# Kernel tuning notes

Measured on AMD Instinct MI355X. Metric: run time of the kernel, lower is better.

Reference implementation:

```python
import jax, jax.numpy as jnp
import numpy as np

B, S, D = 2, 2048, 1024
H, HD = 16, 64
ROPE_BASE = 1000.0


def rope(x):
    # x: [B, H, S, hd]; interleaved (GPT-NeoX-style pairs) rotary embedding, base=1000
    d = x.shape[-1]
    theta = 1.0 / (ROPE_BASE ** (jnp.arange(0, d, 2, dtype=jnp.float32) / d))  # [d/2]
    theta = jnp.repeat(theta, 2)                                               # [d]
    pos = jnp.arange(x.shape[-2], dtype=jnp.float32)                           # [S]
    pm = pos[:, None] * theta[None, :]                                         # [S, d]
    cos, sin = jnp.cos(pm), jnp.sin(pm)
    # rotated: _x[..., 0::2] = -x[..., 1::2]; _x[..., 1::2] = x[..., 0::2]
    rot = jnp.stack([-x[..., 1::2], x[..., 0::2]], axis=-1).reshape(x.shape)
    return x * cos + rot * sin


def setup_inputs() -> dict:
    key = jax.random.key(0)
    ks = jax.random.split(key, 12)
    sc = 1.0 / np.sqrt(D)
    inp = {
        "query": jax.random.normal(ks[0], (B, S, D), jnp.float32),
        "key": jax.random.normal(ks[1], (B, S, D), jnp.float32),
        "value": jax.random.normal(ks[2], (B, S, D), jnp.float32),
        "mask": jnp.broadcast_to(jnp.tril(jnp.ones((S, S), jnp.int32)), (B, S, S)),
        "Wq": jax.random.normal(ks[3], (D, H * HD), jnp.float32) * sc,
        "bq": jax.random.normal(ks[4], (H * HD,), jnp.float32) * 0.01,
        "Wk": jax.random.normal(ks[5], (D, H * HD), jnp.float32) * sc,
        "bk": jax.random.normal(ks[6], (H * HD,), jnp.float32) * 0.01,
        "Wv": jax.random.normal(ks[7], (D, H * HD), jnp.float32) * sc,
        "bv": jax.random.normal(ks[8], (H * HD,), jnp.float32) * 0.01,
        "Wo": jax.random.normal(ks[9], (H * HD, D), jnp.float32) * sc,
        "bo": jax.random.normal(ks[10], (D,), jnp.float32) * 0.01,
    }
    return inp


def reference(query, key, value, mask, Wq, bq, Wk, bk, Wv, bv, Wo, bo):
    b = query.shape[0]
    split = lambda t: t.reshape(b, -1, H, HD).transpose(0, 2, 1, 3)  # [B,H,S,hd]
    q = split(query @ Wq + bq)
    k = split(key @ Wk + bk)
    v = split(value @ Wv + bv)
    qr, kr = rope(q), rope(k)
    scale = jnp.sqrt(jnp.float32(HD))
    num = jnp.exp(jnp.einsum("bhqd,bhkd->bhqk", qr, kr) / scale)           # [B,H,S,S]
    den = jnp.sum(jnp.exp(jnp.einsum("bhqd,bhkd->bhqk", q, k) / scale),
                  axis=-1, keepdims=True)                                   # [B,H,S,1]
    a = num / den
    a = jnp.where(mask[:, None, :, :] == 0, -jnp.inf, a)
    alpha = jax.nn.softmax(a, axis=-1)
    z = jnp.einsum("bhqk,bhkd->bhqd", alpha, v)
    z = z.transpose(0, 2, 1, 3).reshape(b, -1, H * HD)
    return z @ Wo + bo
```

## Files before the change

### kernel.cpp

```cpp
#include <hip/hip_runtime.h>


#define Bn 2
#define Sn 2048
#define Dn 1024
#define Hn 16
#define HDn 64

typedef __attribute__((ext_vector_type(8))) short bf16x8;
typedef __attribute__((ext_vector_type(8))) unsigned short u16x8;
typedef __attribute__((ext_vector_type(4))) unsigned short u16x4;
typedef __attribute__((ext_vector_type(4))) float f32x4;

#define MFMA(a, b, c) __builtin_amdgcn_mfma_f32_16x16x32_bf16(a, b, c, 0, 0, 0)
#define Z4 ((f32x4){0.f, 0.f, 0.f, 0.f})

#define PRESC 0.18033688011112042f
#define C2 0.5287663729448977f

#define EXP2(x) __builtin_amdgcn_exp2f(x)
#define LOG2(x) __builtin_amdgcn_logf(x)

__device__ __forceinline__ unsigned short f2bf(float f) {
  unsigned int u = __builtin_bit_cast(unsigned int, f);
  u = (u + 0x7fffu + ((u >> 16) & 1u)) >> 16;
  return (unsigned short)u;
}

__device__ __forceinline__ unsigned int cvtpk(float lo, float hi) {
  unsigned int r;
  asm("v_cvt_pk_bf16_f32 %0, %1, %2" : "=v"(r) : "v"(lo), "v"(hi));
  return r;
}

__device__ __forceinline__ void gll16(const unsigned short* g, unsigned short* l) {
  __builtin_amdgcn_global_load_lds((const __attribute__((address_space(1))) void*)g,
                                   (__attribute__((address_space(3))) void*)l, 16, 0, 0);
}

#define FR(T, row, x) (*(const bf16x8*)&(T)[(row) * 64 + (((x) ^ ((row) & 7)) * 8)])

__global__ __launch_bounds__(256) void k_trig(float2* __restrict__ T) {
  int idx = blockIdx.x * 256 + threadIdx.x;
  int s = idx >> 5, i = idx & 31;
  float theta = powf(1000.f, -(float)i / 32.f);
  float pm = (float)s * theta;
  T[idx] = make_float2(cosf(pm), sinf(pm));
}

__global__ __launch_bounds__(256) void k_wtrans(
    const float* __restrict__ W0, const float* __restrict__ W1,
    const float* __restrict__ W2, const float* __restrict__ W3,
    unsigned short* __restrict__ O0, unsigned short* __restrict__ O1,
    unsigned short* __restrict__ O2, unsigned short* __restrict__ O3) {
  __shared__ float t[64][65];
  int which = blockIdx.z;
  const float* W = (which == 0) ? W0 : (which == 1) ? W1 : (which == 2) ? W2 : W3;
  unsigned short* O = (which == 0) ? O0 : (which == 1) ? O1 : (which == 2) ? O2 : O3;
  int kb = blockIdx.x * 64, nb = blockIdx.y * 64;
  int tid = threadIdx.x;
#pragma unroll
  for (int rep = 0; rep < 16; ++rep) {
    int e = rep * 256 + tid;
    int k = e >> 6, n = e & 63;
    t[k][n] = W[(kb + k) * Dn + nb + n];
  }
  __syncthreads();
#pragma unroll
  for (int rep = 0; rep < 16; ++rep) {
    int e = rep * 256 + tid;
    int n = e >> 6, k = e & 63;
    O[(nb + n) * Dn + kb + k] = f2bf(t[k][n]);
  }
}

__global__ __launch_bounds__(256) void k_cvt(
    const float* __restrict__ q, const float* __restrict__ k, const float* __restrict__ v,
    unsigned short* __restrict__ oq, unsigned short* __restrict__ ok,
    unsigned short* __restrict__ ov) {
  int z = blockIdx.y;
  const float* s = (z == 0) ? q : (z == 1) ? k : v;
  unsigned short* d = (z == 0) ? oq : (z == 1) ? ok : ov;
  size_t idx = ((size_t)blockIdx.x * 256 + threadIdx.x) * 8;
  float4 a = *(const float4*)(s + idx);
  float4 b = *(const float4*)(s + idx + 4);
  u16x8 pk;
  pk[0] = f2bf(a.x); pk[1] = f2bf(a.y); pk[2] = f2bf(a.z); pk[3] = f2bf(a.w);
  pk[4] = f2bf(b.x); pk[5] = f2bf(b.y); pk[6] = f2bf(b.z); pk[7] = f2bf(b.w);
  *(u16x8*)(d + idx) = pk;
}

__global__ __launch_bounds__(256) void k_gemm_proj(
    const unsigned short* __restrict__ Qa, const unsigned short* __restrict__ Ka,
    const unsigned short* __restrict__ Va,
    const unsigned short* __restrict__ Wq, const unsigned short* __restrict__ Wk,
    const unsigned short* __restrict__ Wv,
    const float* __restrict__ bqp, const float* __restrict__ bkp, const float* __restrict__ bvp,
    const float2* __restrict__ trig,
    unsigned short* __restrict__ Qb, unsigned short* __restrict__ Kb,
    unsigned short* __restrict__ Qr, unsigned short* __restrict__ Kr,
    unsigned short* __restrict__ Vt) {
  __shared__ unsigned short Al[128 * 64];
  __shared__ unsigned short Bl[128 * 64];
  const int tid = threadIdx.x;
  const int wave = tid >> 6, lane = tid & 63, g = lane >> 4, li = lane & 15;
  const int mbase = blockIdx.x * 128, nbase = blockIdx.y * 128;
  const int wm = wave >> 1, wn = wave & 1;
  const int which = blockIdx.z;
  const unsigned short* A = (which == 0) ? Qa : (which == 1) ? Ka : Va;
  const unsigned short* Wt = (which == 0) ? Wq : (which == 1) ? Wk : Wv;
  const float* bias = (which == 0) ? bqp : (which == 1) ? bkp : bvp;

  f32x4 acc[4][4];
#pragma unroll
  for (int i = 0; i < 4; ++i)
#pragma unroll
    for (int j = 0; j < 4; ++j) acc[i][j] = Z4;

  float bv4[4];
#pragma unroll
  for (int nt = 0; nt < 4; ++nt) bv4[nt] = bias[nbase + wn * 64 + nt * 16 + li];

  const int lr8 = lane >> 3, lc = lane & 7;
  const int xc8 = (lc ^ lr8) * 8;
  const unsigned short* srcA = A + (size_t)(mbase + wave * 32 + lr8) * Dn + xc8;
  const unsigned short* srcB = Wt + (size_t)(nbase + wave * 32 + lr8) * Dn + xc8;

  for (int kb = 0; kb < Dn; kb += 64) {
    __syncthreads();
#pragma unroll
    for (int i = 0; i < 4; ++i) {
      gll16(srcA + kb + (size_t)i * (8 * Dn), &Al[(wave * 32 + i * 8) * 64]);
      gll16(srcB + kb + (size_t)i * (8 * Dn), &Bl[(wave * 32 + i * 8) * 64]);
    }
    __syncthreads();
#pragma unroll
    for (int kc = 0; kc < 2; ++kc) {
      bf16x8 af[4], bfr[4];
#pragma unroll
      for (int mt = 0; mt < 4; ++mt) af[mt] = FR(Al, wm * 64 + mt * 16 + li, kc * 4 + g);
#pragma unroll
      for (int nt = 0; nt < 4; ++nt) bfr[nt] = FR(Bl, wn * 64 + nt * 16 + li, kc * 4 + g);
#pragma unroll
      for (int mt = 0; mt < 4; ++mt)
#pragma unroll
        for (int nt = 0; nt < 4; ++nt)
          acc[mt][nt] = MFMA(af[mt], bfr[nt], acc[mt][nt]);
    }
  }

  if (which < 2) {
    unsigned short* Ob = (which == 0) ? Qb : Kb;
    unsigned short* Or = (which == 0) ? Qr : Kr;
    const float presc = (which == 0) ? PRESC : 1.f;
#pragma unroll
    for (int mt = 0; mt < 4; ++mt) {
#pragma unroll
      for (int nt = 0; nt < 4; ++nt) {
        const int n = nbase + wn * 64 + nt * 16 + li;
        const int h = n >> 6, hd = n & 63;
        const int ti = hd >> 1;
        const float sgn = (hd & 1) ? 1.f : -1.f;
#pragma unroll
        for (int r = 0; r < 4; ++r) {
          const int m = mbase + wm * 64 + mt * 16 + 4 * g + r;
          const int b = m >> 11, s = m & (Sn - 1);
          const float v = (acc[mt][nt][r] + bv4[nt]) * presc;
          const size_t oi = (((size_t)(b * Hn + h)) * Sn + s) * HDn + hd;
          Ob[oi] = f2bf(v);
          const float p = __shfl_xor(v, 1);
          const float2 cs = trig[(s << 5) + ti];
          Or[oi] = f2bf(fmaf(sgn * p, cs.y, v * cs.x));
        }
      }
    }
  } else {
#pragma unroll
    for (int mt = 0; mt < 4; ++mt) {
#pragma unroll
      for (int nt = 0; nt < 4; ++nt) {
        const int n = nbase + wn * 64 + nt * 16 + li;
        const int h = n >> 6, hd = n & 63;
        const int m0 = mbase + wm * 64 + mt * 16 + 4 * g;
        const int b = m0 >> 11, s0 = m0 & (Sn - 1);
        u16x4 pk;
#pragma unroll
        for (int r = 0; r < 4; ++r) pk[r] = f2bf(acc[mt][nt][r] + bv4[nt]);
        *(u16x4*)&Vt[(((size_t)(b * Hn + h)) * HDn + hd) * Sn + s0] = pk;
      }
    }
  }
}

__global__ __launch_bounds__(256) void k_gemm_out(const unsigned short* __restrict__ A,
                                                  const unsigned short* __restrict__ Wt,
                                                  const float* __restrict__ bias,
                                                  float* __restrict__ out) {
  __shared__ unsigned short Al[64 * 64];
  __shared__ unsigned short Bl[128 * 64];
  const int tid = threadIdx.x;
  const int wave = tid >> 6, lane = tid & 63, g = lane >> 4, li = lane & 15;
  const int mbase = blockIdx.x * 64, nbase = blockIdx.y * 128;
  const int wm = wave >> 1, wn = wave & 1;

  f32x4 acc[2][4];
#pragma unroll
  for (int i = 0; i < 2; ++i)
#pragma unroll
    for (int j = 0; j < 4; ++j) acc[i][j] = Z4;

  float bv4[4];
#pragma unroll
  for (int nt = 0; nt < 4; ++nt) bv4[nt] = bias[nbase + wn * 64 + nt * 16 + li];

  const int lr8 = lane >> 3, lc = lane & 7;
  const int xc8 = (lc ^ lr8) * 8;
  const unsigned short* srcA = A + (size_t)(mbase + wave * 16 + lr8) * Dn + xc8;
  const unsigned short* srcB = Wt + (size_t)(nbase + wave * 32 + lr8) * Dn + xc8;

  for (int kb = 0; kb < Dn; kb += 64) {
    __syncthreads();
#pragma unroll
    for (int i = 0; i < 2; ++i)
      gll16(srcA + kb + (size_t)i * (8 * Dn), &Al[(wave * 16 + i * 8) * 64]);
#pragma unroll
    for (int i = 0; i < 4; ++i)
      gll16(srcB + kb + (size_t)i * (8 * Dn), &Bl[(wave * 32 + i * 8) * 64]);
    __syncthreads();
#pragma unroll
    for (int kc = 0; kc < 2; ++kc) {
      bf16x8 af[2], bfr[4];
#pragma unroll
      for (int mt = 0; mt < 2; ++mt) af[mt] = FR(Al, wm * 32 + mt * 16 + li, kc * 4 + g);
#pragma unroll
      for (int nt = 0; nt < 4; ++nt) bfr[nt] = FR(Bl, wn * 64 + nt * 16 + li, kc * 4 + g);
#pragma unroll
      for (int mt = 0; mt < 2; ++mt)
#pragma unroll
        for (int nt = 0; nt < 4; ++nt)
          acc[mt][nt] = MFMA(af[mt], bfr[nt], acc[mt][nt]);
    }
  }

#pragma unroll
  for (int mt = 0; mt < 2; ++mt)
#pragma unroll
    for (int nt = 0; nt < 4; ++nt) {
      const int n = nbase + wn * 64 + nt * 16 + li;
#pragma unroll
      for (int r = 0; r < 4; ++r) {
        const int m = mbase + wm * 32 + mt * 16 + 4 * g + r;
        out[(size_t)m * Dn + n] = acc[mt][nt][r] + bv4[nt];
      }
    }
}

__global__ __launch_bounds__(256, 4) void k_attn(
    const unsigned short* __restrict__ Qr, const unsigned short* __restrict__ Kr,
    const unsigned short* __restrict__ Qb, const unsigned short* __restrict__ Kb,
    const unsigned short* __restrict__ Vt, unsigned short* __restrict__ Zb) {
  __shared__ unsigned short KT[2][8192];
  __shared__ unsigned short Pl[4][1024];

  const int tid = threadIdx.x;
  const int wave = tid >> 6, lane = tid & 63, g = lane >> 4, li = lane & 15;
  const int bid = blockIdx.x;
  const int i4 = bid & 3, j = bid >> 2;
  const int bh = j & 31, grp = j >> 5;
  const int qt = (i4 == 0) ? grp : (i4 == 1) ? 15 - grp : (i4 == 2) ? 16 + grp : 31 - grp;
  const int qw = qt * 64 + wave * 16;
  const size_t kvbase = (size_t)bh * (Sn * HDn);

  bf16x8 qrf[2], qbf[2];
#pragma unroll
  for (int kc = 0; kc < 2; ++kc) {
    const size_t a = kvbase + (size_t)(qw + li) * HDn + kc * 32 + g * 8;
    qrf[kc] = *(const bf16x8*)(Qr + a);
    qbf[kc] = *(const bf16x8*)(Qb + a);
  }

  const int lr8 = lane >> 3, lc = lane & 7;
  const int xc8 = (lc ^ lr8) * 8;

  const unsigned short* srcPA = Kb + kvbase + (size_t)(wave * 32 + lr8) * HDn + xc8;
  const int tw = wave >> 1, rbB = (wave & 1) * 32;
  const unsigned short* srcKrB = Kr + kvbase + (size_t)(rbB + lr8) * HDn + xc8;
  const unsigned short* srcVtB = Vt + kvbase + (size_t)(rbB + lr8) * Sn + xc8;
  const size_t strIB = tw ? (size_t)(8 * Sn) : (size_t)(8 * HDn);
  unsigned short* myP = &Pl[wave][0];

  bool dm[4];
#pragma unroll
  for (int r = 0; r < 4; ++r) dm[r] = (4 * g + r) <= li;

#define STAGE_PA(kb_, buf_)                                 \
  do {                                                      \
    unsigned short* d_ = &KT[buf_][(wave * 32) * 64];       \
    const unsigned short* s_ = srcPA + (size_t)(kb_)*HDn;   \
    gll16(s_, d_);                                          \
    gll16(s_ + 8 * HDn, d_ + 8 * 64);                       \
    gll16(s_ + 16 * HDn, d_ + 16 * 64);                     \
    gll16(s_ + 24 * HDn, d_ + 24 * 64);                     \
  } while (0)

#define STAGE_B(kb_, buf_)                                                    \
  do {                                                                        \
    unsigned short* d_ = &KT[buf_][tw * 4096 + rbB * 64];                     \
    const unsigned short* s_ =                                                \
        tw ? (srcVtB + (size_t)(kb_)) : (srcKrB + (size_t)(kb_)*HDn);         \
    gll16(s_, d_);                                                            \
    gll16(s_ + strIB, d_ + 8 * 64);                                           \
    gll16(s_ + 2 * strIB, d_ + 16 * 64);                                      \
    gll16(s_ + 3 * strIB, d_ + 24 * 64);                                      \
  } while (0)

  float d4[4] = {0.f, 0.f, 0.f, 0.f};
  STAGE_PA(0, 0);
  __syncthreads();
  for (int t = 0; t < Sn / 128; ++t) {
    if (t + 1 < Sn / 128) STAGE_PA((t + 1) * 128, (t + 1) & 1);
    const unsigned short* TK = &KT[t & 1][0];
#pragma unroll
    for (int nt = 0; nt < 8; ++nt) {
      const int krow = nt * 16 + li;
      const bf16x8 kf0 = FR(TK, krow, g), kf1 = FR(TK, krow, 4 + g);
      f32x4 s = Z4;
      s = MFMA(kf0, qbf[0], s);
      s = MFMA(kf1, qbf[1], s);
#pragma unroll
      for (int r = 0; r < 4; ++r) d4[r] += EXP2(s[r]);
    }
    __syncthreads();
  }
  float den = (d4[0] + d4[1]) + (d4[2] + d4[3]);
  den += __shfl_xor(den, 16);
  den += __shfl_xor(den, 32);
  const float Lc = LOG2(den) - C2;
  const f32x4 mLc = {-Lc, -Lc, -Lc, -Lc};

  f32x4 accz[4];
#pragma unroll
  for (int i = 0; i < 4; ++i) accz[i] = Z4;
  float ws[4] = {0.f, 0.f, 0.f, 0.f};
  const int NTB = qt + 1;

  STAGE_B(0, 0);
  __syncthreads();
  for (int t = 0; t < NTB; ++t) {
    if (t + 1 < NTB) STAGE_B((t + 1) * 64, (t + 1) & 1);
    const unsigned short* T0 = &KT[t & 1][0];
    const unsigned short* TV = &KT[t & 1][0] + 4096;
    const bool last = (t == qt);
#pragma unroll
    for (int nt = 0; nt < 4; ++nt) {
      float w[4];
      if (!last || nt <= wave) {
        const int krow = nt * 16 + li;
        const bf16x8 kf0 = FR(T0, krow, g), kf1 = FR(T0, krow, 4 + g);
        f32x4 s = mLc;
        s = MFMA(kf0, qrf[0], s);
        s = MFMA(kf1, qrf[1], s);
        if (last && nt == wave) {
#pragma unroll
          for (int r = 0; r < 4; ++r) {
            const float e = EXP2(EXP2(s[r]));
            w[r] = dm[r] ? e : 0.f;
            ws[r] += w[r];
          }
        } else {
#pragma unroll
          for (int r = 0; r < 4; ++r) {
            w[r] = EXP2(EXP2(s[r]));
            ws[r] += w[r];
          }
        }
      } else {
        w[0] = w[1] = w[2] = w[3] = 0.f;
      }
      const int adr = li * 64 + (((nt * 2 + (g >> 1)) ^ (li & 7)) * 8) + (g & 1) * 4;
      *(uint2*)&myP[adr] = (uint2){cvtpk(w[0], w[1]), cvtpk(w[2], w[3])};
    }
#pragma unroll
    for (int kc = 0; kc < 2; ++kc) {
      const bf16x8 pa = FR(myP, li, kc * 4 + g);
#pragma unroll
      for (int n2 = 0; n2 < 4; ++n2) {
        const bf16x8 vb = FR(TV, n2 * 16 + li, kc * 4 + g);
        accz[n2] = MFMA(pa, vb, accz[n2]);
      }
    }
    __syncthreads();
  }

  float wsum = (ws[0] + ws[1]) + (ws[2] + ws[3]);
  wsum += __shfl_xor(wsum, 16);
  wsum += __shfl_xor(wsum, 32);
  float rw[4];
#pragma unroll
  for (int r = 0; r < 4; ++r) rw[r] = 1.f / __shfl(wsum, 4 * g + r);
  const int b = bh >> 4, h = bh & 15;
#pragma unroll
  for (int n2 = 0; n2 < 4; ++n2) {
#pragma unroll
    for (int r = 0; r < 4; ++r) {
      const int hd = n2 * 16 + li;
      const int q = qw + 4 * g + r;
      Zb[((size_t)(b * Sn + q)) * Dn + h * HDn + hd] = f2bf(accz[n2][r] * rw[r]);
    }
  }
#undef STAGE_PA
#undef STAGE_B
}

extern "C" void kernel_launch(void* const* d_in, const int* in_sizes, int n_in,
                              void* d_out, int out_size, void* d_ws, size_t ws_size,
                              hipStream_t stream) {
  const float* query = (const float*)d_in[0];
  const float* key   = (const float*)d_in[1];
  const float* value = (const float*)d_in[2];
  const float* Wq = (const float*)d_in[4];
  const float* bq = (const float*)d_in[5];
  const float* Wk = (const float*)d_in[6];
  const float* bk = (const float*)d_in[7];
  const float* Wv = (const float*)d_in[8];
  const float* bv = (const float*)d_in[9];
  const float* Wo = (const float*)d_in[10];
  const float* bo = (const float*)d_in[11];

  char* ws = (char*)d_ws;
  const size_t MB = 1ull << 20;
  unsigned short* Wqt = (unsigned short*)(ws + 0 * MB);
  unsigned short* Wkt = (unsigned short*)(ws + 2 * MB);
  unsigned short* Wvt = (unsigned short*)(ws + 4 * MB);
  unsigned short* Wot = (unsigned short*)(ws + 6 * MB);
  float2* trig        = (float2*)(ws + 8 * MB);
  unsigned short* Qa  = (unsigned short*)(ws + 9 * MB);
  unsigned short* Ka  = (unsigned short*)(ws + 17 * MB);
  unsigned short* Va  = (unsigned short*)(ws + 25 * MB);
  unsigned short* Qb  = (unsigned short*)(ws + 33 * MB);
  unsigned short* Kb  = (unsigned short*)(ws + 41 * MB);
  unsigned short* Qr  = (unsigned short*)(ws + 49 * MB);
  unsigned short* Kr  = (unsigned short*)(ws + 57 * MB);
  unsigned short* Vt  = (unsigned short*)(ws + 65 * MB);
  unsigned short* Zb  = (unsigned short*)(ws + 73 * MB);

  k_trig<<<256, 256, 0, stream>>>(trig);
  k_wtrans<<<dim3(16, 16, 4), 256, 0, stream>>>(Wq, Wk, Wv, Wo, Wqt, Wkt, Wvt, Wot);
  k_cvt<<<dim3(2048, 3), 256, 0, stream>>>(query, key, value, Qa, Ka, Va);
  k_gemm_proj<<<dim3(32, 8, 3), 256, 0, stream>>>(Qa, Ka, Va, Wqt, Wkt, Wvt,
                                                  bq, bk, bv, trig, Qb, Kb, Qr, Kr, Vt);
  k_attn<<<1024, 256, 0, stream>>>(Qr, Kr, Qb, Kb, Vt, Zb);
  k_gemm_out<<<dim3(64, 8), 256, 0, stream>>>(Zb, Wot, bo, (float*)d_out);
}
```

Baseline: 157.8 us.

## Split denominator pass into own kernel, pair causal q-tiles, merge prep kernels

```diff
diff --git a/kernel.cpp b/kernel.cpp
--- a/kernel.cpp
+++ b/kernel.cpp
@@ -40,54 +40,55 @@
 
 #define FR(T, row, x) (*(const bf16x8*)&(T)[(row) * 64 + (((x) ^ ((row) & 7)) * 8)])
 
-__global__ __launch_bounds__(256) void k_trig(float2* __restrict__ T) {
-  int idx = blockIdx.x * 256 + threadIdx.x;
-  int s = idx >> 5, i = idx & 31;
-  float theta = powf(1000.f, -(float)i / 32.f);
-  float pm = (float)s * theta;
-  T[idx] = make_float2(cosf(pm), sinf(pm));
-}
-
-__global__ __launch_bounds__(256) void k_wtrans(
+__global__ __launch_bounds__(256) void k_pre(
     const float* __restrict__ W0, const float* __restrict__ W1,
     const float* __restrict__ W2, const float* __restrict__ W3,
     unsigned short* __restrict__ O0, unsigned short* __restrict__ O1,
-    unsigned short* __restrict__ O2, unsigned short* __restrict__ O3) {
+    unsigned short* __restrict__ O2, unsigned short* __restrict__ O3,
+    const float* __restrict__ qa, const float* __restrict__ ka, const float* __restrict__ va,
+    unsigned short* __restrict__ oq, unsigned short* __restrict__ ok,
+    unsigned short* __restrict__ ov, float2* __restrict__ T) {
   __shared__ float t[64][65];
-  int which = blockIdx.z;
-  const float* W = (which == 0) ? W0 : (which == 1) ? W1 : (which == 2) ? W2 : W3;
-  unsigned short* O = (which == 0) ? O0 : (which == 1) ? O1 : (which == 2) ? O2 : O3;
-  int kb = blockIdx.x * 64, nb = blockIdx.y * 64;
-  int tid = threadIdx.x;
-#pragma unroll
-  for (int rep = 0; rep < 16; ++rep) {
-    int e = rep * 256 + tid;
-    int k = e >> 6, n = e & 63;
-    t[k][n] = W[(kb + k) * Dn + nb + n];
-  }
-  __syncthreads();
-#pragma unroll
-  for (int rep = 0; rep < 16; ++rep) {
-    int e = rep * 256 + tid;
-    int n = e >> 6, k = e & 63;
-    O[(nb + n) * Dn + kb + k] = f2bf(t[k][n]);
-  }
-}
-
-__global__ __launch_bounds__(256) void k_cvt(
-    const float* __restrict__ q, const float* __restrict__ k, const float* __restrict__ v,
-    unsigned short* __restrict__ oq, unsigned short* __restrict__ ok,
-    unsigned short* __restrict__ ov) {
-  int z = blockIdx.y;
-  const float* s = (z == 0) ? q : (z == 1) ? k : v;
-  unsigned short* d = (z == 0) ? oq : (z == 1) ? ok : ov;
-  size_t idx = ((size_t)blockIdx.x * 256 + threadIdx.x) * 8;
-  float4 a = *(const float4*)(s + idx);
-  float4 b = *(const float4*)(s + idx + 4);
-  u16x8 pk;
-  pk[0] = f2bf(a.x); pk[1] = f2bf(a.y); pk[2] = f2bf(a.z); pk[3] = f2bf(a.w);
-  pk[4] = f2bf(b.x); pk[5] = f2bf(b.y); pk[6] = f2bf(b.z); pk[7] = f2bf(b.w);
-  *(u16x8*)(d + idx) = pk;
+  const int b = blockIdx.x;
+  const int tid = threadIdx.x;
+  if (b < 256) {
+    const int idx = b * 256 + tid;
+    const int s = idx >> 5, i = idx & 31;
+    const float theta = powf(1000.f, -(float)i / 32.f);
+    const float pm = (float)s * theta;
+    T[idx] = make_float2(cosf(pm), sinf(pm));
+  } else if (b < 1280) {
+    const int w = b - 256;
+    const int which = w >> 8, rem = w & 255;
+    const float* W = (which == 0) ? W0 : (which == 1) ? W1 : (which == 2) ? W2 : W3;
+    unsigned short* O = (which == 0) ? O0 : (which == 1) ? O1 : (which == 2) ? O2 : O3;
+    const int kb = (rem >> 4) * 64, nb = (rem & 15) * 64;
+#pragma unroll
+    for (int rep = 0; rep < 16; ++rep) {
+      const int e = rep * 256 + tid;
+      const int k = e >> 6, n = e & 63;
+      t[k][n] = W[(kb + k) * Dn + nb + n];
+    }
+    __syncthreads();
+#pragma unroll
+    for (int rep = 0; rep < 16; ++rep) {
+      const int e = rep * 256 + tid;
+      const int n = e >> 6, k = e & 63;
+      O[(nb + n) * Dn + kb + k] = f2bf(t[k][n]);
+    }
+  } else {
+    const int c = b - 1280;
+    const int z = c >> 11, cx = c & 2047;
+    const float* s = (z == 0) ? qa : (z == 1) ? ka : va;
+    unsigned short* d = (z == 0) ? oq : (z == 1) ? ok : ov;
+    const size_t idx = ((size_t)cx * 256 + tid) * 8;
+    float4 a0 = *(const float4*)(s + idx);
+    float4 b0 = *(const float4*)(s + idx + 4);
+    u16x8 pk;
+    pk[0] = f2bf(a0.x); pk[1] = f2bf(a0.y); pk[2] = f2bf(a0.z); pk[3] = f2bf(a0.w);
+    pk[4] = f2bf(b0.x); pk[5] = f2bf(b0.y); pk[6] = f2bf(b0.z); pk[7] = f2bf(b0.w);
+    *(u16x8*)(d + idx) = pk;
+  }
 }
 
 __global__ __launch_bounds__(256) void k_gemm_proj(
@@ -255,161 +256,243 @@
     }
 }
 
-__global__ __launch_bounds__(256, 4) void k_attn(
-    const unsigned short* __restrict__ Qr, const unsigned short* __restrict__ Kr,
-    const unsigned short* __restrict__ Qb, const unsigned short* __restrict__ Kb,
-    const unsigned short* __restrict__ Vt, unsigned short* __restrict__ Zb) {
-  __shared__ unsigned short KT[2][8192];
-  __shared__ unsigned short Pl[4][1024];
+__global__ __launch_bounds__(128, 4) void k_den(const unsigned short* __restrict__ Qb,
+                                                const unsigned short* __restrict__ Kb,
+                                                float* __restrict__ Lbuf) {
+  __shared__ unsigned short KT[2][128 * 64];
 
   const int tid = threadIdx.x;
   const int wave = tid >> 6, lane = tid & 63, g = lane >> 4, li = lane & 15;
-  const int bid = blockIdx.x;
-  const int i4 = bid & 3, j = bid >> 2;
-  const int bh = j & 31, grp = j >> 5;
-  const int qt = (i4 == 0) ? grp : (i4 == 1) ? 15 - grp : (i4 == 2) ? 16 + grp : 31 - grp;
-  const int qw = qt * 64 + wave * 16;
+  const int raw = blockIdx.x;
+  const int xcd = raw & 7, idx = raw >> 3;
+  const int bh = xcd * 4 + (idx >> 4);
+  const int qb = idx & 15;
+  const int q0 = qb * 128 + wave * 64;
   const size_t kvbase = (size_t)bh * (Sn * HDn);
 
-  bf16x8 qrf[2], qbf[2];
-#pragma unroll
-  for (int kc = 0; kc < 2; ++kc) {
-    const size_t a = kvbase + (size_t)(qw + li) * HDn + kc * 32 + g * 8;
-    qrf[kc] = *(const bf16x8*)(Qr + a);
-    qbf[kc] = *(const bf16x8*)(Qb + a);
-  }
+  bf16x8 qbf[4][2];
+#pragma unroll
+  for (int j = 0; j < 4; ++j)
+#pragma unroll
+    for (int kc = 0; kc < 2; ++kc)
+      qbf[j][kc] = *(const bf16x8*)(Qb + kvbase + (size_t)(q0 + j * 16 + li) * HDn + kc * 32 + g * 8);
 
   const int lr8 = lane >> 3, lc = lane & 7;
   const int xc8 = (lc ^ lr8) * 8;
-
-  const unsigned short* srcPA = Kb + kvbase + (size_t)(wave * 32 + lr8) * HDn + xc8;
-  const int tw = wave >> 1, rbB = (wave & 1) * 32;
-  const unsigned short* srcKrB = Kr + kvbase + (size_t)(rbB + lr8) * HDn + xc8;
-  const unsigned short* srcVtB = Vt + kvbase + (size_t)(rbB + lr8) * Sn + xc8;
-  const size_t strIB = tw ? (size_t)(8 * Sn) : (size_t)(8 * HDn);
-  unsigned short* myP = &Pl[wave][0];
-
-  bool dm[4];
-#pragma unroll
-  for (int r = 0; r < 4; ++r) dm[r] = (4 * g + r) <= li;
-
-#define STAGE_PA(kb_, buf_)                                 \
-  do {                                                      \
-    unsigned short* d_ = &KT[buf_][(wave * 32) * 64];       \
-    const unsigned short* s_ = srcPA + (size_t)(kb_)*HDn;   \
-    gll16(s_, d_);                                          \
-    gll16(s_ + 8 * HDn, d_ + 8 * 64);                       \
-    gll16(s_ + 16 * HDn, d_ + 16 * 64);                     \
-    gll16(s_ + 24 * HDn, d_ + 24 * 64);                     \
+  const unsigned short* src = Kb + kvbase + (size_t)(wave * 64 + lr8) * HDn + xc8;
+
+#define STG(kb_, buf_)                                                        \
+  do {                                                                        \
+    _Pragma("unroll") for (int i = 0; i < 8; ++i)                             \
+        gll16(src + (size_t)((kb_) + i * 8) * HDn, &KT[buf_][(wave * 64 + i * 8) * 64]); \
   } while (0)
 
-#define STAGE_B(kb_, buf_)                                                    \
-  do {                                                                        \
-    unsigned short* d_ = &KT[buf_][tw * 4096 + rbB * 64];                     \
-    const unsigned short* s_ =                                                \
-        tw ? (srcVtB + (size_t)(kb_)) : (srcKrB + (size_t)(kb_)*HDn);         \
-    gll16(s_, d_);                                                            \
-    gll16(s_ + strIB, d_ + 8 * 64);                                           \
-    gll16(s_ + 2 * strIB, d_ + 16 * 64);                                      \
-    gll16(s_ + 3 * strIB, d_ + 24 * 64);                                      \
-  } while (0)
-
-  float d4[4] = {0.f, 0.f, 0.f, 0.f};
-  STAGE_PA(0, 0);
+  float dacc[4][4];
+#pragma unroll
+  for (int j = 0; j < 4; ++j)
+#pragma unroll
+    for (int r = 0; r < 4; ++r) dacc[j][r] = 0.f;
+
+  STG(0, 0);
   __syncthreads();
   for (int t = 0; t < Sn / 128; ++t) {
-    if (t + 1 < Sn / 128) STAGE_PA((t + 1) * 128, (t + 1) & 1);
+    if (t + 1 < Sn / 128) STG((t + 1) * 128, (t + 1) & 1);
     const unsigned short* TK = &KT[t & 1][0];
 #pragma unroll
     for (int nt = 0; nt < 8; ++nt) {
       const int krow = nt * 16 + li;
       const bf16x8 kf0 = FR(TK, krow, g), kf1 = FR(TK, krow, 4 + g);
-      f32x4 s = Z4;
-      s = MFMA(kf0, qbf[0], s);
-      s = MFMA(kf1, qbf[1], s);
-#pragma unroll
-      for (int r = 0; r < 4; ++r) d4[r] += EXP2(s[r]);
-    }
-    __syncthreads();
-  }
-  float den = (d4[0] + d4[1]) + (d4[2] + d4[3]);
-  den += __shfl_xor(den, 16);
-  den += __shfl_xor(den, 32);
-  const float Lc = LOG2(den) - C2;
-  const f32x4 mLc = {-Lc, -Lc, -Lc, -Lc};
-
-  f32x4 accz[4];
-#pragma unroll
-  for (int i = 0; i < 4; ++i) accz[i] = Z4;
-  float ws[4] = {0.f, 0.f, 0.f, 0.f};
-  const int NTB = qt + 1;
-
-  STAGE_B(0, 0);
+#pragma unroll
+      for (int j = 0; j < 4; ++j) {
+        f32x4 s = Z4;
+        s = MFMA(kf0, qbf[j][0], s);
+        s = MFMA(kf1, qbf[j][1], s);
+#pragma unroll
+        for (int r = 0; r < 4; ++r) dacc[j][r] += EXP2(s[r]);
+      }
+    }
+    __syncthreads();
+  }
+#pragma unroll
+  for (int j = 0; j < 4; ++j) {
+    float den = (dacc[j][0] + dacc[j][1]) + (dacc[j][2] + dacc[j][3]);
+    den += __shfl_xor(den, 16);
+    den += __shfl_xor(den, 32);
+    if (lane < 16) Lbuf[bh * Sn + q0 + j * 16 + li] = LOG2(den) - C2;
+  }
+#undef STG
+}
+
+__global__ __launch_bounds__(256, 2) void k_attn(
+    const unsigned short* __restrict__ Qr, const unsigned short* __restrict__ Kr,
+    const unsigned short* __restrict__ Vt, const float* __restrict__ Lbuf,
+    unsigned short* __restrict__ Zb) {
+  __shared__ unsigned short KT[2][64 * 64];
+  __shared__ unsigned short Pl[4][2][1024];
+
+  const int tid = threadIdx.x;
+  const int wave = tid >> 6, lane = tid & 63, g = lane >> 4, li = lane & 15;
+  const int raw = blockIdx.x;
+  const int xcd = raw & 7, idx = raw >> 3;
+  const int bh = xcd * 4 + (idx >> 4);
+  const int f = idx & 15;
+  const int tL = f, tH = 31 - f;
+  const int qwL = tL * 64 + wave * 16, qwH = tH * 64 + wave * 16;
+  const size_t kvbase = (size_t)bh * (Sn * HDn);
+
+  bf16x8 qrfL[2], qrfH[2];
+#pragma unroll
+  for (int kc = 0; kc < 2; ++kc) {
+    qrfL[kc] = *(const bf16x8*)(Qr + kvbase + (size_t)(qwL + li) * HDn + kc * 32 + g * 8);
+    qrfH[kc] = *(const bf16x8*)(Qr + kvbase + (size_t)(qwH + li) * HDn + kc * 32 + g * 8);
+  }
+  const float mLcL = -Lbuf[bh * Sn + qwL + li];
+  const float mLcH = -Lbuf[bh * Sn + qwH + li];
+
+  const int lr8 = lane >> 3, lc = lane & 7;
+  const int xc8 = (lc ^ lr8) * 8;
+  const unsigned short* srcK = Kr + kvbase + (size_t)(wave * 16 + lr8) * HDn + xc8;
+
+#define STGK(kb_, buf_)                                                      \
+  do {                                                                       \
+    gll16(srcK + (size_t)(kb_)*HDn, &KT[buf_][(wave * 16) * 64]);            \
+    gll16(srcK + (size_t)((kb_) + 8) * HDn, &KT[buf_][(wave * 16 + 8) * 64]); \
+  } while (0)
+
+  const unsigned short* vp0 = Vt + kvbase + (size_t)(0 * 16 + li) * Sn + g * 8;
+  const unsigned short* vp1 = Vt + kvbase + (size_t)(1 * 16 + li) * Sn + g * 8;
+  const unsigned short* vp2 = Vt + kvbase + (size_t)(2 * 16 + li) * Sn + g * 8;
+  const unsigned short* vp3 = Vt + kvbase + (size_t)(3 * 16 + li) * Sn + g * 8;
+
+  unsigned short* myPL = &Pl[wave][0][0];
+  unsigned short* myPH = &Pl[wave][1][0];
+
+  f32x4 acczL[4], acczH[4];
+#pragma unroll
+  for (int i = 0; i < 4; ++i) {
+    acczL[i] = Z4;
+    acczH[i] = Z4;
+  }
+  float wsL[4] = {0.f, 0.f, 0.f, 0.f}, wsH[4] = {0.f, 0.f, 0.f, 0.f};
+  bool dm[4];
+#pragma unroll
+  for (int r = 0; r < 4; ++r) dm[r] = (4 * g + r) <= li;
+
+  STGK(0, 0);
   __syncthreads();
-  for (int t = 0; t < NTB; ++t) {
-    if (t + 1 < NTB) STAGE_B((t + 1) * 64, (t + 1) & 1);
+  for (int t = 0; t <= tH; ++t) {
+    if (t < tH) STGK((t + 1) * 64, (t + 1) & 1);
+    bf16x8 v00 = *(const bf16x8*)(vp0 + t * 64);
+    bf16x8 v01 = *(const bf16x8*)(vp1 + t * 64);
+    bf16x8 v02 = *(const bf16x8*)(vp2 + t * 64);
+    bf16x8 v03 = *(const bf16x8*)(vp3 + t * 64);
+    bf16x8 v10 = *(const bf16x8*)(vp0 + t * 64 + 32);
+    bf16x8 v11 = *(const bf16x8*)(vp1 + t * 64 + 32);
+    bf16x8 v12 = *(const bf16x8*)(vp2 + t * 64 + 32);
+    bf16x8 v13 = *(const bf16x8*)(vp3 + t * 64 + 32);
+
     const unsigned short* T0 = &KT[t & 1][0];
-    const unsigned short* TV = &KT[t & 1][0] + 4096;
-    const bool last = (t == qt);
+    const bool loAct = (t <= tL);
 #pragma unroll
     for (int nt = 0; nt < 4; ++nt) {
-      float w[4];
-      if (!last || nt <= wave) {
-        const int krow = nt * 16 + li;
-        const bf16x8 kf0 = FR(T0, krow, g), kf1 = FR(T0, krow, 4 + g);
-        f32x4 s = mLc;
-        s = MFMA(kf0, qrf[0], s);
-        s = MFMA(kf1, qrf[1], s);
-        if (last && nt == wave) {
-#pragma unroll
-          for (int r = 0; r < 4; ++r) {
-            const float e = EXP2(EXP2(s[r]));
-            w[r] = dm[r] ? e : 0.f;
-            ws[r] += w[r];
+      const int krow = nt * 16 + li;
+      const bf16x8 kf0 = FR(T0, krow, g), kf1 = FR(T0, krow, 4 + g);
+      const int adr = li * 64 + (((nt * 2 + (g >> 1)) ^ (li & 7)) * 8) + (g & 1) * 4;
+      {
+        float w[4];
+        if (t < tH || nt <= wave) {
+          f32x4 s = {mLcH, mLcH, mLcH, mLcH};
+          s = MFMA(kf0, qrfH[0], s);
+          s = MFMA(kf1, qrfH[1], s);
+          if (t == tH && nt == wave) {
+#pragma unroll
+            for (int r = 0; r < 4; ++r) {
+              const float e = EXP2(EXP2(s[r]));
+              w[r] = dm[r] ? e : 0.f;
+            }
+          } else {
+#pragma unroll
+            for (int r = 0; r < 4; ++r) w[r] = EXP2(EXP2(s[r]));
           }
+#pragma unroll
+          for (int r = 0; r < 4; ++r) wsH[r] += w[r];
         } else {
-#pragma unroll
-          for (int r = 0; r < 4; ++r) {
-            w[r] = EXP2(EXP2(s[r]));
-            ws[r] += w[r];
+          w[0] = w[1] = w[2] = w[3] = 0.f;
+        }
+        *(uint2*)&myPH[adr] = (uint2){cvtpk(w[0], w[1]), cvtpk(w[2], w[3])};
+      }
+      if (loAct) {
+        float w[4];
+        if (t < tL || nt <= wave) {
+          f32x4 s = {mLcL, mLcL, mLcL, mLcL};
+          s = MFMA(kf0, qrfL[0], s);
+          s = MFMA(kf1, qrfL[1], s);
+          if (t == tL && nt == wave) {
+#pragma unroll
+            for (int r = 0; r < 4; ++r) {
+              const float e = EXP2(EXP2(s[r]));
+              w[r] = dm[r] ? e : 0.f;
+            }
+          } else {
+#pragma unroll
+            for (int r = 0; r < 4; ++r) w[r] = EXP2(EXP2(s[r]));
           }
+#pragma unroll
+          for (int r = 0; r < 4; ++r) wsL[r] += w[r];
+        } else {
+          w[0] = w[1] = w[2] = w[3] = 0.f;
         }
-      } else {
-        w[0] = w[1] = w[2] = w[3] = 0.f;
-      }
-      const int adr = li * 64 + (((nt * 2 + (g >> 1)) ^ (li & 7)) * 8) + (g & 1) * 4;
-      *(uint2*)&myP[adr] = (uint2){cvtpk(w[0], w[1]), cvtpk(w[2], w[3])};
-    }
-#pragma unroll
-    for (int kc = 0; kc < 2; ++kc) {
-      const bf16x8 pa = FR(myP, li, kc * 4 + g);
-#pragma unroll
-      for (int n2 = 0; n2 < 4; ++n2) {
-        const bf16x8 vb = FR(TV, n2 * 16 + li, kc * 4 + g);
-        accz[n2] = MFMA(pa, vb, accz[n2]);
-      }
-    }
-    __syncthreads();
-  }
-
-  float wsum = (ws[0] + ws[1]) + (ws[2] + ws[3]);
-  wsum += __shfl_xor(wsum, 16);
-  wsum += __shfl_xor(wsum, 32);
-  float rw[4];
-#pragma unroll
-  for (int r = 0; r < 4; ++r) rw[r] = 1.f / __shfl(wsum, 4 * g + r);
+        *(uint2*)&myPL[adr] = (uint2){cvtpk(w[0], w[1]), cvtpk(w[2], w[3])};
+      }
+    }
+    {
+      const bf16x8 paH0 = FR(myPH, li, 0 + g), paH1 = FR(myPH, li, 4 + g);
+      acczH[0] = MFMA(paH0, v00, acczH[0]);
+      acczH[1] = MFMA(paH0, v01, acczH[1]);
+      acczH[2] = MFMA(paH0, v02, acczH[2]);
+      acczH[3] = MFMA(paH0, v03, acczH[3]);
+      acczH[0] = MFMA(paH1, v10, acczH[0]);
+      acczH[1] = MFMA(paH1, v11, acczH[1]);
+      acczH[2] = MFMA(paH1, v12, acczH[2]);
+      acczH[3] = MFMA(paH1, v13, acczH[3]);
+      if (loAct) {
+        const bf16x8 paL0 = FR(myPL, li, 0 + g), paL1 = FR(myPL, li, 4 + g);
+        acczL[0] = MFMA(paL0, v00, acczL[0]);
+        acczL[1] = MFMA(paL0, v01, acczL[1]);
+        acczL[2] = MFMA(paL0, v02, acczL[2]);
+        acczL[3] = MFMA(paL0, v03, acczL[3]);
+        acczL[0] = MFMA(paL1, v10, acczL[0]);
+        acczL[1] = MFMA(paL1, v11, acczL[1]);
+        acczL[2] = MFMA(paL1, v12, acczL[2]);
+        acczL[3] = MFMA(paL1, v13, acczL[3]);
+      }
+    }
+    __syncthreads();
+  }
+
+  float wsumL = (wsL[0] + wsL[1]) + (wsL[2] + wsL[3]);
+  float wsumH = (wsH[0] + wsH[1]) + (wsH[2] + wsH[3]);
+  wsumL += __shfl_xor(wsumL, 16);
+  wsumL += __shfl_xor(wsumL, 32);
+  wsumH += __shfl_xor(wsumH, 16);
+  wsumH += __shfl_xor(wsumH, 32);
+  float rwL[4], rwH[4];
+#pragma unroll
+  for (int r = 0; r < 4; ++r) {
+    rwL[r] = 1.f / __shfl(wsumL, 4 * g + r);
+    rwH[r] = 1.f / __shfl(wsumH, 4 * g + r);
+  }
   const int b = bh >> 4, h = bh & 15;
 #pragma unroll
   for (int n2 = 0; n2 < 4; ++n2) {
 #pragma unroll
     for (int r = 0; r < 4; ++r) {
       const int hd = n2 * 16 + li;
-      const int q = qw + 4 * g + r;
-      Zb[((size_t)(b * Sn + q)) * Dn + h * HDn + hd] = f2bf(accz[n2][r] * rw[r]);
-    }
-  }
-#undef STAGE_PA
-#undef STAGE_B
+      Zb[((size_t)(b * Sn + qwL + 4 * g + r)) * Dn + h * HDn + hd] = f2bf(acczL[n2][r] * rwL[r]);
+      Zb[((size_t)(b * Sn + qwH + 4 * g + r)) * Dn + h * HDn + hd] = f2bf(acczH[n2][r] * rwH[r]);
+    }
+  }
+#undef STGK
 }
 
 extern "C" void kernel_launch(void* const* d_in, const int* in_sizes, int n_in,
@@ -434,6 +517,7 @@
   unsigned short* Wvt = (unsigned short*)(ws + 4 * MB);
   unsigned short* Wot = (unsigned short*)(ws + 6 * MB);
   float2* trig        = (float2*)(ws + 8 * MB);
+  float* Lbuf         = (float*)(ws + 8 * MB + 512 * 1024);
   unsigned short* Qa  = (unsigned short*)(ws + 9 * MB);
   unsigned short* Ka  = (unsigned short*)(ws + 17 * MB);
   unsigned short* Va  = (unsigned short*)(ws + 25 * MB);
@@ -444,11 +528,11 @@
   unsigned short* Vt  = (unsigned short*)(ws + 65 * MB);
   unsigned short* Zb  = (unsigned short*)(ws + 73 * MB);
 
-  k_trig<<<256, 256, 0, stream>>>(trig);
-  k_wtrans<<<dim3(16, 16, 4), 256, 0, stream>>>(Wq, Wk, Wv, Wo, Wqt, Wkt, Wvt, Wot);
-  k_cvt<<<dim3(2048, 3), 256, 0, stream>>>(query, key, value, Qa, Ka, Va);
+  k_pre<<<7424, 256, 0, stream>>>(Wq, Wk, Wv, Wo, Wqt, Wkt, Wvt, Wot,
+                                  query, key, value, Qa, Ka, Va, trig);
   k_gemm_proj<<<dim3(32, 8, 3), 256, 0, stream>>>(Qa, Ka, Va, Wqt, Wkt, Wvt,
                                                   bq, bk, bv, trig, Qb, Kb, Qr, Kr, Vt);
-  k_attn<<<1024, 256, 0, stream>>>(Qr, Kr, Qb, Kb, Vt, Zb);
+  k_den<<<512, 128, 0, stream>>>(Qb, Kb, Lbuf);
+  k_attn<<<512, 256, 0, stream>>>(Qr, Kr, Vt, Lbuf, Zb);
   k_gemm_out<<<dim3(64, 8), 256, 0, stream>>>(Zb, Wot, bo, (float*)d_out);
 }
```

Result: slower. 185.2 us (+17.4%).
